# Kernel tuning notes

Measured on AMD Instinct MI355X. Metric: run time of the kernel, lower is better.

The kernel has to match this reference:

```python
import jax, jax.numpy as jnp
import numpy as np

DEGREE = 8
IN_FEATURES = 256
OUT_FEATURES = 256
BATCH = 2048


def setup_inputs() -> dict:
    key = jax.random.key(0)
    k1, k2, k3 = jax.random.split(key, 3)
    x = jax.random.normal(k1, (BATCH, IN_FEATURES), dtype=jnp.float32)
    # VarianceScaling(scale=1.0, fan_in) default: truncated normal ~ stddev sqrt(1/fan_in); plain normal is fine for a numeric reference
    base_weight = jax.random.normal(k2, (IN_FEATURES, OUT_FEATURES), dtype=jnp.float32) * (1.0 / np.sqrt(IN_FEATURES))
    cheb_weight = jax.random.normal(k3, (IN_FEATURES, OUT_FEATURES, DEGREE), dtype=jnp.float32) * (1.0 / np.sqrt(IN_FEATURES))
    return {"x": x, "base_weight": base_weight, "cheb_weight": cheb_weight}


def _chebyshev_basis(x, degree):
    # global min/max rescale to [-1, 1] over the WHOLE tensor (as in the TF source)
    xmin = jnp.min(x)
    xmax = jnp.max(x)
    xs = 2.0 * (x - xmin) / (xmax - xmin) - 1.0
    T = [jnp.ones_like(xs), xs]
    for _ in range(2, degree):
        T.append(2.0 * xs * T[-1] - T[-2])
    return jnp.stack(T, axis=-1)  # (batch, in, degree)


def reference(x, base_weight, cheb_weight):
    # base path: swish(x) @ W_base -> (batch, out)
    base_out = jnp.matmul(x * jax.nn.sigmoid(x), base_weight)
    # cheb path: contract only over degree axis (faithful to reduce_sum(axis=-1))
    basis = _chebyshev_basis(x, DEGREE)  # (b, i, d)
    cheb_out = jnp.einsum('bid,iod->bio', basis, cheb_weight)  # (b, i, o)
    # broadcast add: (b, 1, o) + (b, i, o) -> (b, i, o)
    return base_out[:, None, :] + cheb_out
```

## Files before the change

### kernel.cpp

```cpp
#include <hip/hip_runtime.h>
#include <math.h>

#define BATCH 2048
#define IN_F 256
#define OUT_F 256
#define DEG 8

typedef __attribute__((ext_vector_type(4))) float f4;


__global__ __launch_bounds__(256) void k_minmax_partial(const float* __restrict__ x,
                                                        float* __restrict__ ws) {
    int t = threadIdx.x;
    int blk = blockIdx.x;
    const f4* x4 = (const f4*)x;
    float mn = 1e30f, mx = -1e30f;
    int base = blk * 2048 + t;
#pragma unroll
    for (int j = 0; j < 8; ++j) {
        f4 v = x4[base + j * 256];
        mn = fminf(mn, fminf(fminf(v.x, v.y), fminf(v.z, v.w)));
        mx = fmaxf(mx, fmaxf(fmaxf(v.x, v.y), fmaxf(v.z, v.w)));
    }
#pragma unroll
    for (int off = 32; off > 0; off >>= 1) {
        mn = fminf(mn, __shfl_down(mn, off));
        mx = fmaxf(mx, __shfl_down(mx, off));
    }
    __shared__ float smn[4], smx[4];
    if ((t & 63) == 0) { smn[t >> 6] = mn; smx[t >> 6] = mx; }
    __syncthreads();
    if (t == 0) {
        mn = fminf(fminf(smn[0], smn[1]), fminf(smn[2], smn[3]));
        mx = fmaxf(fmaxf(smx[0], smx[1]), fmaxf(smx[2], smx[3]));
        ws[blk] = mn;
        ws[64 + blk] = mx;
    }
}

__global__ void k_minmax_final(float* __restrict__ ws) {
    int t = threadIdx.x;
    float mn = ws[t], mx = ws[64 + t];
#pragma unroll
    for (int off = 32; off > 0; off >>= 1) {
        mn = fminf(mn, __shfl_down(mn, off));
        mx = fmaxf(mx, __shfl_down(mx, off));
    }
    if (t == 0) {
        float a = 2.0f / (mx - mn);
        ws[128] = a;
        ws[129] = -a * mn - 1.0f;
    }
}

#define KC 64
__global__ __launch_bounds__(256) void k_base(const float* __restrict__ x,
                                              const float* __restrict__ w,
                                              float* __restrict__ basews) {
    __shared__ float As[32][KC + 1];
    __shared__ float Bs[KC][64];
    int t = threadIdx.x;
    int b0 = blockIdx.x * 32;
    int o0 = blockIdx.y * 64;
    int to = t & 15;
    int tb = t >> 4;
    f4 acc0 = {0.f, 0.f, 0.f, 0.f}, acc1 = {0.f, 0.f, 0.f, 0.f};
    for (int kc = 0; kc < IN_F; kc += KC) {
        __syncthreads();
#pragma unroll
        for (int j = 0; j < 2; ++j) {
            int e = t + 256 * j;
            int b = e >> 4;
            int k4 = e & 15;
            f4 v = ((const f4*)(x + (size_t)(b0 + b) * IN_F + kc))[k4];
            v.x = v.x / (1.0f + __expf(-v.x));
            v.y = v.y / (1.0f + __expf(-v.y));
            v.z = v.z / (1.0f + __expf(-v.z));
            v.w = v.w / (1.0f + __expf(-v.w));
            As[b][k4 * 4 + 0] = v.x;
            As[b][k4 * 4 + 1] = v.y;
            As[b][k4 * 4 + 2] = v.z;
            As[b][k4 * 4 + 3] = v.w;
        }
#pragma unroll
        for (int j = 0; j < 4; ++j) {
            int e = t + 256 * j;
            int k = e >> 4;
            int o4 = e & 15;
            f4 v = ((const f4*)(w + (size_t)(kc + k) * OUT_F + o0))[o4];
            *((f4*)&Bs[k][o4 * 4]) = v;
        }
        __syncthreads();
#pragma unroll 8
        for (int k = 0; k < KC; ++k) {
            float a0 = As[2 * tb][k];
            float a1 = As[2 * tb + 1][k];
            f4 bv = *((const f4*)&Bs[k][to * 4]);
            acc0 += a0 * bv;
            acc1 += a1 * bv;
        }
    }
    float* dst = basews + (size_t)(b0 + 2 * tb) * OUT_F + o0 + to * 4;
    *((f4*)dst) = acc0;
    *((f4*)(dst + OUT_F)) = acc1;
}

__global__ __launch_bounds__(256) void k_main(const float* __restrict__ x,
                                              const float* __restrict__ cw,
                                              const float* __restrict__ basews,
                                              const float* __restrict__ scl,
                                              float* __restrict__ out) {
    int t = threadIdx.x;
    int to = t & 15;
    int ig = t >> 4;
    int i0 = blockIdx.x * 16;
    int o0 = blockIdx.y * 64;
    int b0 = blockIdx.z * 32;
    float a = scl[0];
    float c = scl[1];
    int i = i0 + ig;

    const f4* wsrc = (const f4*)(cw + ((size_t)i * OUT_F + (o0 + to * 4)) * DEG);
    float wv[4][8];
#pragma unroll
    for (int ol = 0; ol < 4; ++ol) {
        f4 lo = wsrc[ol * 2];
        f4 hi = wsrc[ol * 2 + 1];
        wv[ol][0] = lo.x; wv[ol][1] = lo.y; wv[ol][2] = lo.z; wv[ol][3] = lo.w;
        wv[ol][4] = hi.x; wv[ol][5] = hi.y; wv[ol][6] = hi.z; wv[ol][7] = hi.w;
    }

    const float* xp = x + (size_t)b0 * IN_F + i;
    const float* bp = basews + (size_t)b0 * OUT_F + o0 + to * 4;
    float* op = out + ((size_t)b0 * IN_F + i) * OUT_F + o0 + to * 4;

    for (int bb = 0; bb < 32; ++bb) {
        float xv = xp[(size_t)bb * IN_F];
        float xs = fmaf(a, xv, c);
        float T[8];
        T[0] = 1.0f;
        T[1] = xs;
        float x2 = xs + xs;
#pragma unroll
        for (int d = 2; d < DEG; ++d) T[d] = fmaf(x2, T[d - 1], -T[d - 2]);

        f4 r = *(const f4*)(bp + (size_t)bb * OUT_F);
#pragma unroll
        for (int d = 0; d < DEG; ++d) {
            r.x = fmaf(T[d], wv[0][d], r.x);
            r.y = fmaf(T[d], wv[1][d], r.y);
            r.z = fmaf(T[d], wv[2][d], r.z);
            r.w = fmaf(T[d], wv[3][d], r.w);
        }
        __builtin_nontemporal_store(r, (f4*)(op + (size_t)bb * IN_F * OUT_F));
    }
}

extern "C" void kernel_launch(void* const* d_in, const int* in_sizes, int n_in,
                              void* d_out, int out_size, void* d_ws, size_t ws_size,
                              hipStream_t stream) {
    (void)in_sizes; (void)n_in; (void)out_size; (void)ws_size;
    const float* x  = (const float*)d_in[0];
    const float* bw = (const float*)d_in[1];
    const float* cw = (const float*)d_in[2];
    float* out = (float*)d_out;
    float* ws = (float*)d_ws;
    float* scl = ws + 128;
    float* basews = ws + 256;

    k_minmax_partial<<<64, 256, 0, stream>>>(x, ws);
    k_minmax_final<<<1, 64, 0, stream>>>(ws);
    dim3 gb(BATCH / 32, OUT_F / 64);
    k_base<<<gb, 256, 0, stream>>>(x, bw, basews);
    dim3 gm(IN_F / 16, OUT_F / 64, BATCH / 32);
    k_main<<<gm, 256, 0, stream>>>(x, cw, basews, scl, out);
}
```

Baseline: 545.0 us.

## Remap k_main so each wavefront covers full output row for two inputs

k_main is reorganized so each wavefront handles two input features across all 256 outputs, with each lane owning 4 consecutive outputs. Each base vector load is shared by both features, and each wave writes full contiguous 1 KB rows. The grid drops the output-tile dimension, giving fewer, larger blocks. Weight registers per thread double to 64 floats, which may lower occupancy. The weight load stride per lane is also larger than before.

```diff
diff --git a/kernel.cpp b/kernel.cpp
--- a/kernel.cpp
+++ b/kernel.cpp
@@ -111,48 +111,67 @@
                                               const float* __restrict__ scl,
                                               float* __restrict__ out) {
     int t = threadIdx.x;
-    int to = t & 15;
-    int ig = t >> 4;
-    int i0 = blockIdx.x * 16;
-    int o0 = blockIdx.y * 64;
-    int b0 = blockIdx.z * 32;
+    int l = t & 63;
+    int wv = t >> 6;
+    int i0 = blockIdx.x * 8;
+    int b0 = blockIdx.y * 32;
+    int ia = i0 + 2 * wv;
+    int ib = ia + 1;
     float a = scl[0];
     float c = scl[1];
-    int i = i0 + ig;
 
-    const f4* wsrc = (const f4*)(cw + ((size_t)i * OUT_F + (o0 + to * 4)) * DEG);
-    float wv[4][8];
+    const f4* wpa = (const f4*)(cw + (size_t)ia * (OUT_F * DEG) + (size_t)l * 32);
+    const f4* wpb = (const f4*)(cw + (size_t)ib * (OUT_F * DEG) + (size_t)l * 32);
+    float wa[32], wb[32];
 #pragma unroll
-    for (int ol = 0; ol < 4; ++ol) {
-        f4 lo = wsrc[ol * 2];
-        f4 hi = wsrc[ol * 2 + 1];
-        wv[ol][0] = lo.x; wv[ol][1] = lo.y; wv[ol][2] = lo.z; wv[ol][3] = lo.w;
-        wv[ol][4] = hi.x; wv[ol][5] = hi.y; wv[ol][6] = hi.z; wv[ol][7] = hi.w;
+    for (int j = 0; j < 8; ++j) {
+        f4 va = wpa[j];
+        wa[4 * j + 0] = va.x; wa[4 * j + 1] = va.y;
+        wa[4 * j + 2] = va.z; wa[4 * j + 3] = va.w;
+        f4 vb = wpb[j];
+        wb[4 * j + 0] = vb.x; wb[4 * j + 1] = vb.y;
+        wb[4 * j + 2] = vb.z; wb[4 * j + 3] = vb.w;
     }
 
-    const float* xp = x + (size_t)b0 * IN_F + i;
-    const float* bp = basews + (size_t)b0 * OUT_F + o0 + to * 4;
-    float* op = out + ((size_t)b0 * IN_F + i) * OUT_F + o0 + to * 4;
+    const float* xpa = x + (size_t)b0 * IN_F + ia;
+    const float* xpb = x + (size_t)b0 * IN_F + ib;
+    const f4* bp = (const f4*)(basews + (size_t)b0 * OUT_F) + l;
+    f4* opa = (f4*)(out + ((size_t)b0 * IN_F + ia) * OUT_F) + l;
+    f4* opb = (f4*)(out + ((size_t)b0 * IN_F + ib) * OUT_F) + l;
 
+#pragma unroll 2
     for (int bb = 0; bb < 32; ++bb) {
-        float xv = xp[(size_t)bb * IN_F];
-        float xs = fmaf(a, xv, c);
-        float T[8];
-        T[0] = 1.0f;
-        T[1] = xs;
-        float x2 = xs + xs;
+        float xva = xpa[(size_t)bb * IN_F];
+        float xvb = xpb[(size_t)bb * IN_F];
+        f4 base = bp[(size_t)bb * (OUT_F / 4)];
+
+        float xsa = fmaf(a, xva, c);
+        float xsb = fmaf(a, xvb, c);
+        float Ta[8], Tb[8];
+        Ta[0] = 1.0f; Ta[1] = xsa;
+        Tb[0] = 1.0f; Tb[1] = xsb;
+        float x2a = xsa + xsa;
+        float x2b = xsb + xsb;
 #pragma unroll
-        for (int d = 2; d < DEG; ++d) T[d] = fmaf(x2, T[d - 1], -T[d - 2]);
+        for (int d = 2; d < DEG; ++d) {
+            Ta[d] = fmaf(x2a, Ta[d - 1], -Ta[d - 2]);
+            Tb[d] = fmaf(x2b, Tb[d - 1], -Tb[d - 2]);
+        }
 
-        f4 r = *(const f4*)(bp + (size_t)bb * OUT_F);
+        f4 ra = base, rb = base;
 #pragma unroll
         for (int d = 0; d < DEG; ++d) {
-            r.x = fmaf(T[d], wv[0][d], r.x);
-            r.y = fmaf(T[d], wv[1][d], r.y);
-            r.z = fmaf(T[d], wv[2][d], r.z);
-            r.w = fmaf(T[d], wv[3][d], r.w);
+            ra.x = fmaf(Ta[d], wa[0 + d], ra.x);
+            ra.y = fmaf(Ta[d], wa[8 + d], ra.y);
+            ra.z = fmaf(Ta[d], wa[16 + d], ra.z);
+            ra.w = fmaf(Ta[d], wa[24 + d], ra.w);
+            rb.x = fmaf(Tb[d], wb[0 + d], rb.x);
+            rb.y = fmaf(Tb[d], wb[8 + d], rb.y);
+            rb.z = fmaf(Tb[d], wb[16 + d], rb.z);
+            rb.w = fmaf(Tb[d], wb[24 + d], rb.w);
         }
-        __builtin_nontemporal_store(r, (f4*)(op + (size_t)bb * IN_F * OUT_F));
+        __builtin_nontemporal_store(ra, opa + (size_t)bb * (IN_F * OUT_F / 4));
+        __builtin_nontemporal_store(rb, opb + (size_t)bb * (IN_F * OUT_F / 4));
     }
 }
 
@@ -172,6 +191,6 @@
     k_minmax_final<<<1, 64, 0, stream>>>(ws);
     dim3 gb(BATCH / 32, OUT_F / 64);
     k_base<<<gb, 256, 0, stream>>>(x, bw, basews);
-    dim3 gm(IN_F / 16, OUT_F / 64, BATCH / 32);
+    dim3 gm(IN_F / 8, BATCH / 32);
     k_main<<<gm, 256, 0, stream>>>(x, cw, basews, scl, out);
 }
```

Measured after the change: 550.2 us. Within noise of the previous version (+0.9%).
